# Kernel optimization log

Measured on AMD Instinct MI355X. Metric: run time of the kernel, lower is better.

Reference implementation:

```python
import jax, jax.numpy as jnp
import numpy as np

L, B, S, D, H, DH, V = 6, 2048, 64, 256, 8, 64, 100
INNER = H * DH          # 512
FF = 4 * D              # 1024 (GeGLU hidden after chunk)
SCALE = 8.0             # sqrt(DH)


def setup_inputs() -> dict:
    key = jax.random.key(0)
    ks = jax.random.split(key, 8)
    s = 0.02
    return {
        "x": jax.random.randint(ks[0], (B, S), 0, V),
        "E": jax.random.normal(ks[1], (S, V, D), dtype=jnp.float32) * s,
        "ln1_g": jnp.ones((L, D), jnp.float32),
        "ln1_b": jnp.zeros((L, D), jnp.float32),
        "Wqkv": jax.random.normal(ks[2], (L, D, 3 * INNER), dtype=jnp.float32) * s,
        "Wout": jax.random.normal(ks[3], (L, INNER, D), dtype=jnp.float32) * s,
        "bout": jnp.zeros((L, D), jnp.float32),
        "ln2_g": jnp.ones((L, D), jnp.float32),
        "ln2_b": jnp.zeros((L, D), jnp.float32),
        "W1": jax.random.normal(ks[4], (L, D, 2 * FF), dtype=jnp.float32) * s,
        "b1": jnp.zeros((L, 2 * FF), jnp.float32),
        "W2": jax.random.normal(ks[5], (L, FF, D), dtype=jnp.float32) * s,
        "b2": jnp.zeros((L, D), jnp.float32),
    }


def _ln(x, g, b):
    m = x.mean(-1, keepdims=True)
    v = ((x - m) ** 2).mean(-1, keepdims=True)
    return (x - m) * jax.lax.rsqrt(v + 1e-5) * g + b


def _split_heads(t):
    # [B,S,H*DH] -> [B,H,S,DH]
    return t.reshape(B, S, H, DH).transpose(0, 2, 1, 3)


def reference(x, E, ln1_g, ln1_b, Wqkv, Wout, bout, ln2_g, ln2_b, W1, b1, W2, b2):
    # per-column embedding lookup: E[col, x[b,col]] -> [B,S,D]
    h = E[jnp.arange(S)[None, :], x]
    for l in range(L):
        # PreNorm -> MHA
        n = _ln(h, ln1_g[l], ln1_b[l])
        qkv = n @ Wqkv[l]
        q, k, v = jnp.split(qkv, 3, axis=-1)
        q, k, v = _split_heads(q), _split_heads(k), _split_heads(v)
        score = jax.nn.softmax(
            jnp.einsum("bhqd,bhkd->bhqk", q, k) / SCALE, axis=-1
        )
        o = jnp.einsum("bhqk,bhkd->bhqd", score, v)
        o = o.transpose(0, 2, 1, 3).reshape(B, S, INNER)
        h = h + o @ Wout[l] + bout[l]
        # PreNorm -> GeGLU FFN
        n2 = _ln(h, ln2_g[l], ln2_b[l])
        u = n2 @ W1[l] + b1[l]
        a, g = jnp.split(u, 2, axis=-1)
        h = (a * jax.nn.gelu(g, approximate=False)) @ W2[l] + b2[l] + h
    return h
```

## Files before the change

### kernel.cpp

```cpp
#include <hip/hip_runtime.h>
#include <stdint.h>
#include <math.h>


#define LAYERS 6
#define BATCH  2048
#define SEQ    64
#define DMODEL 256
#define NHEAD  8
#define INNERD 512
#define FFDIM  1024
#define VOCAB  100
#define MTOK   (BATCH*SEQ)

typedef unsigned short u16;
typedef __attribute__((ext_vector_type(4))) float f32x4;
typedef __attribute__((ext_vector_type(4))) short s16x4;
typedef __attribute__((ext_vector_type(8))) short s16x8;

__device__ inline u16 f2bf(float f){
  union { float f; unsigned int u; } x; x.f = f;
  unsigned int u = x.u;
  return (u16)((u + 0x7fffu + ((u >> 16) & 1u)) >> 16);
}

__device__ inline void gload16(const void* g, void* l){
  __builtin_amdgcn_global_load_lds(
      (const __attribute__((address_space(1))) unsigned int*)g,
      (__attribute__((address_space(3))) unsigned int*)l, 16, 0, 0);
}

__device__ inline f32x4 mfma16(s16x8 a, s16x8 b, f32x4 c){
  return __builtin_amdgcn_mfma_f32_16x16x32_bf16(a, b, c, 0, 0, 0);
}

__device__ inline s16x8 ldfrag(const u16* lds, int row, int kk, int g){
  int chunk = ((kk<<2)|g) ^ (row&7);
  return *(const s16x8*)(lds + row*64 + chunk*8);
}

__device__ inline int pcol32(int col_base32, int hi, int g, int o){
  return col_base32 | (g<<3) | (hi<<2) | o;
}

__global__ __launch_bounds__(256) void wtrans_kernel(
    const float* __restrict__ in, u16* __restrict__ out, int K, int N, int total)
{
  int idx = blockIdx.x*256 + threadIdx.x;
  if (idx >= total) return;
  int l = idx / (N*K);
  int r = idx - l*(N*K);
  int n = r / K;
  int k = r - n*K;
  int p = (k & ~31) | (((k>>2)&3)<<3) | (((k>>4)&1)<<2) | (k&3);
  out[(size_t)l*N*K + (size_t)n*K + p] = f2bf(in[(size_t)l*K*N + (size_t)k*N + n]);
}

__global__ __launch_bounds__(256) void embed_ln_kernel(
    const int* __restrict__ x, const float* __restrict__ E,
    const float* __restrict__ gam, const float* __restrict__ bet,
    float* __restrict__ h, u16* __restrict__ nout)
{
  int t = threadIdx.x;
  int m = blockIdx.x*4 + (t>>6);
  int lane = t & 63;
  int s = m & 63;
  int tok = x[m];
  const float4 v = *(const float4*)(E + ((size_t)s*VOCAB + tok)*DMODEL + lane*4);
  *(float4*)(h + (size_t)m*DMODEL + lane*4) = v;
  float su = v.x+v.y+v.z+v.w;
  float q  = v.x*v.x+v.y*v.y+v.z*v.z+v.w*v.w;
  #pragma unroll
  for (int mask=1; mask<64; mask<<=1){
    su += __shfl_xor(su, mask);
    q  += __shfl_xor(q,  mask);
  }
  float mean = su*(1.f/256.f);
  float var  = q*(1.f/256.f) - mean*mean;
  float rs   = rsqrtf(var + 1e-5f);
  const float4 gv = *(const float4*)(gam + lane*4);
  const float4 bv = *(const float4*)(bet + lane*4);
  ushort4 ov;
  ov.x = f2bf((v.x-mean)*rs*gv.x + bv.x);
  ov.y = f2bf((v.y-mean)*rs*gv.y + bv.y);
  ov.z = f2bf((v.z-mean)*rs*gv.z + bv.z);
  ov.w = f2bf((v.w-mean)*rs*gv.w + bv.w);
  int p4 = (lane>>3)*32 + (lane&3)*8 + ((lane>>2)&1)*4;
  *(ushort4*)(nout + (size_t)m*DMODEL + p4) = ov;
}

__global__ __launch_bounds__(256, 2) void gemm_qkv_kernel(
    const u16* __restrict__ A, const u16* __restrict__ Bt,
    u16* __restrict__ outb, int K, int N)
{
  __shared__ __align__(16) u16 As[128*64];
  __shared__ __align__(16) u16 Bs[128*64];
  const int t = threadIdx.x;
  const int w = t >> 6, lane = t & 63, g = lane >> 4, c = lane & 15;
  const int nxb = N >> 7;
  const int cpx = gridDim.x >> 3;
  const int wg = (blockIdx.x & 7)*cpx + (blockIdx.x >> 3);
  const int n0 = (wg % nxb) * 128, m0 = (wg / nxb) * 128;
  const int wm = (w >> 1) * 64, wn = (w & 1) * 64;

  f32x4 acc[4][4];
  #pragma unroll
  for (int i=0;i<4;++i)
    #pragma unroll
    for (int j=0;j<4;++j){ f32x4 z = {0.f,0.f,0.f,0.f}; acc[i][j] = z; }

  const int nkt = K >> 6;
  for (int kt = 0; kt < nkt; ++kt){
    #pragma unroll
    for (int i=0;i<4;++i){
      int cid = (i*4 + w)*64 + lane;
      int row = cid >> 3, qs = cid & 7;
      int col16 = ((qs ^ (row&7))<<3);
      gload16(A  + (size_t)(m0+row)*K + (size_t)kt*64 + col16, As + (i*4+w)*512);
      gload16(Bt + (size_t)(n0+row)*K + (size_t)kt*64 + col16, Bs + (i*4+w)*512);
    }
    asm volatile("s_waitcnt vmcnt(0)" ::: "memory");
    __syncthreads();
    #pragma unroll
    for (int kk=0; kk<2; ++kk){
      s16x8 af[4];
      #pragma unroll
      for (int i=0;i<4;++i) af[i] = ldfrag(As, wm + i*16 + c, kk, g);
      #pragma unroll
      for (int j=0;j<4;++j){
        s16x8 bf = ldfrag(Bs, wn + j*16 + c, kk, g);
        #pragma unroll
        for (int i=0;i<4;++i) acc[i][j] = mfma16(af[i], bf, acc[i][j]);
      }
    }
    __syncthreads();
  }

  #pragma unroll
  for (int i=0;i<4;++i)
    #pragma unroll
    for (int j=0;j<4;++j){
      int col = n0 + wn + j*16 + c;
      #pragma unroll
      for (int r=0;r<4;++r){
        int m = m0 + wm + i*16 + g*4 + r;
        outb[(size_t)m*N + col] = f2bf(acc[i][j][r]);
      }
    }
}

__global__ __launch_bounds__(256, 2) void gemm_gated_kernel(
    const u16* __restrict__ A, const u16* __restrict__ Bt,
    u16* __restrict__ act, const float* __restrict__ b1, int K)
{
  __shared__ __align__(16) u16 As[128*64];
  __shared__ __align__(16) u16 Ba[128*64];
  __shared__ __align__(16) u16 Bg[128*64];
  const int t = threadIdx.x;
  const int w = t >> 6, lane = t & 63, g = lane >> 4, c = lane & 15;
  const int cpx = gridDim.x >> 3;
  const int wg = (blockIdx.x & 7)*cpx + (blockIdx.x >> 3);
  const int n0 = (wg & 7) * 128, m0 = (wg >> 3) * 128;
  const int wm = (w >> 1) * 64, wn = (w & 1) * 64;

  f32x4 acca[4][4], accg[4][4];
  #pragma unroll
  for (int i=0;i<4;++i)
    #pragma unroll
    for (int j=0;j<4;++j){ f32x4 z = {0.f,0.f,0.f,0.f}; acca[i][j] = z; accg[i][j] = z; }

  const int nkt = K >> 6;
  for (int kt = 0; kt < nkt; ++kt){
    #pragma unroll
    for (int i=0;i<4;++i){
      int cid = (i*4 + w)*64 + lane;
      int row = cid >> 3, qs = cid & 7;
      int col16 = ((qs ^ (row&7))<<3);
      gload16(A  + (size_t)(m0+row)*K      + (size_t)kt*64 + col16, As + (i*4+w)*512);
      gload16(Bt + (size_t)(n0+row)*K      + (size_t)kt*64 + col16, Ba + (i*4+w)*512);
      gload16(Bt + (size_t)(1024+n0+row)*K + (size_t)kt*64 + col16, Bg + (i*4+w)*512);
    }
    asm volatile("s_waitcnt vmcnt(0)" ::: "memory");
    __syncthreads();
    #pragma unroll
    for (int kk=0; kk<2; ++kk){
      s16x8 af[4];
      #pragma unroll
      for (int i=0;i<4;++i) af[i] = ldfrag(As, wm + i*16 + c, kk, g);
      #pragma unroll
      for (int j=0;j<4;++j){
        int row = wn + j*16 + c;
        s16x8 bfa = ldfrag(Ba, row, kk, g);
        s16x8 bfg = ldfrag(Bg, row, kk, g);
        #pragma unroll
        for (int i=0;i<4;++i){
          acca[i][j] = mfma16(af[i], bfa, acca[i][j]);
          accg[i][j] = mfma16(af[i], bfg, accg[i][j]);
        }
      }
    }
    __syncthreads();
  }

  #pragma unroll
  for (int i=0;i<4;++i)
    #pragma unroll
    for (int j=0;j<4;++j){
      int col = n0 + wn + j*16 + c;
      int pc = pcol32(col & ~31, j&1, c>>2, c&3);
      float ba = b1[col], bg = b1[1024 + col];
      #pragma unroll
      for (int r=0;r<4;++r){
        int m = m0 + wm + i*16 + g*4 + r;
        float ua = acca[i][j][r] + ba;
        float ug = accg[i][j][r] + bg;
        float gel = 0.5f*ug*(1.0f + erff(ug*0.70710678118654752f));
        act[(size_t)m*FFDIM + pc] = f2bf(ua*gel);
      }
    }
}

template<int DO_LN>
__global__ __launch_bounds__(256, 2) void gemm_res_ln_kernel(
    const u16* __restrict__ A, const u16* __restrict__ Bt,
    float* __restrict__ h, const float* __restrict__ bias,
    const float* __restrict__ gam, const float* __restrict__ bet,
    u16* __restrict__ nout, int K)
{
  __shared__ __align__(16) u16 As[128*64];
  __shared__ __align__(16) u16 Bs[256*64];
  __shared__ float ps[128][4];
  const int t = threadIdx.x;
  const int w = t >> 6, lane = t & 63, g = lane >> 4, c = lane & 15;
  const int wr = w >> 1, wc = w & 1;
  const int m0 = blockIdx.x * 128;

  f32x4 acc[4][8];
  #pragma unroll
  for (int i=0;i<4;++i)
    #pragma unroll
    for (int j=0;j<8;++j){ f32x4 z = {0.f,0.f,0.f,0.f}; acc[i][j] = z; }

  const int nkt = K >> 6;
  for (int kt = 0; kt < nkt; ++kt){
    #pragma unroll
    for (int i=0;i<4;++i){
      int cid = (i*4 + w)*64 + lane;
      int row = cid >> 3, qs = cid & 7;
      gload16(A + (size_t)(m0+row)*K + (size_t)kt*64 + ((qs ^ (row&7))<<3),
              As + (i*4+w)*512);
    }
    #pragma unroll
    for (int i=0;i<8;++i){
      int cid = (i*4 + w)*64 + lane;
      int row = cid >> 3, qs = cid & 7;
      gload16(Bt + (size_t)row*K + (size_t)kt*64 + ((qs ^ (row&7))<<3),
              Bs + (i*4+w)*512);
    }
    asm volatile("s_waitcnt vmcnt(0)" ::: "memory");
    __syncthreads();
    #pragma unroll
    for (int kk=0; kk<2; ++kk){
      s16x8 af[4];
      #pragma unroll
      for (int i=0;i<4;++i) af[i] = ldfrag(As, wr*64 + i*16 + c, kk, g);
      #pragma unroll
      for (int j=0;j<8;++j){
        s16x8 bf = ldfrag(Bs, wc*128 + j*16 + c, kk, g);
        #pragma unroll
        for (int i=0;i<4;++i) acc[i][j] = mfma16(af[i], bf, acc[i][j]);
      }
    }
    __syncthreads();
  }

  #pragma unroll
  for (int i=0;i<4;++i){
    #pragma unroll
    for (int r=0;r<4;++r){
      int rl = wr*64 + i*16 + g*4 + r;
      size_t mrow = (size_t)(m0 + rl)*DMODEL;
      float s = 0.f, q2 = 0.f;
      #pragma unroll
      for (int j=0;j<8;++j){
        int col = wc*128 + j*16 + c;
        float v = acc[i][j][r] + bias[col] + h[mrow + col];
        h[mrow + col] = v;
        s += v; q2 += v*v;
      }
      if (DO_LN){
        #pragma unroll
        for (int mask=1; mask<16; mask<<=1){
          s  += __shfl_xor(s,  mask);
          q2 += __shfl_xor(q2, mask);
        }
        if (c == 0){ ps[rl][wc*2] = s; ps[rl][wc*2+1] = q2; }
      }
    }
  }
  if (DO_LN){
    __syncthreads();
    #pragma unroll
    for (int i=0;i<4;++i){
      #pragma unroll
      for (int r=0;r<4;++r){
        int rl = wr*64 + i*16 + g*4 + r;
        size_t mrow = (size_t)(m0 + rl)*DMODEL;
        float st = ps[rl][0] + ps[rl][2];
        float qt = ps[rl][1] + ps[rl][3];
        float mean = st*(1.f/256.f);
        float var  = qt*(1.f/256.f) - mean*mean;
        float rs   = rsqrtf(var + 1e-5f);
        #pragma unroll
        for (int j=0;j<8;++j){
          int col = wc*128 + j*16 + c;
          float v = h[mrow + col];
          int pc = pcol32(col & ~31, j&1, c>>2, c&3);
          nout[mrow + pc] = f2bf((v-mean)*rs*gam[col] + bet[col]);
        }
      }
    }
  }
}

__global__ __launch_bounds__(256) void attn_kernel(
    const u16* __restrict__ qkv, u16* __restrict__ o)
{
  __shared__ __align__(16) u16 qs[64*72];
  __shared__ __align__(16) u16 ks[64*72];
  __shared__ __align__(16) u16 vt[64*72];
  __shared__ __align__(16) u16 psm[4*16*72];
  const int t = threadIdx.x;
  const int w = t >> 6, lane = t & 63, g = lane >> 4, c = lane & 15;
  const int bh = blockIdx.x, b = bh >> 3, hh = bh & 7;
  const size_t qbase = (size_t)b*64*1536 + hh*64;

  #pragma unroll
  for (int i=0;i<2;++i){
    int cid = i*256 + t;
    int row = cid >> 3, seg = cid & 7;
    size_t go = qbase + (size_t)row*1536 + seg*8;
    *(uint4*)(&qs[row*72 + seg*8]) = *(const uint4*)(qkv + go);
    *(uint4*)(&ks[row*72 + seg*8]) = *(const uint4*)(qkv + go + 512);
    uint4 vv = *(const uint4*)(qkv + go + 1024);
    const u16* pv = (const u16*)&vv;
    #pragma unroll
    for (int j=0;j<8;++j) vt[(seg*8+j)*72 + row] = pv[j];
  }
  __syncthreads();

  f32x4 accS[4];
  #pragma unroll
  for (int nf=0;nf<4;++nf){ f32x4 z = {0.f,0.f,0.f,0.f}; accS[nf] = z; }
  const int arow = w*16 + c;
  #pragma unroll
  for (int kk=0;kk<2;++kk){
    int k0 = kk*32 + 4*g;
    s16x4 alo = *(const s16x4*)(qs + arow*72 + k0);
    s16x4 ahi = *(const s16x4*)(qs + arow*72 + k0 + 16);
    s16x8 a = __builtin_shufflevector(alo, ahi, 0,1,2,3,4,5,6,7);
    #pragma unroll
    for (int nf=0;nf<4;++nf){
      int brow = nf*16 + c;
      s16x4 blo = *(const s16x4*)(ks + brow*72 + k0);
      s16x4 bhi = *(const s16x4*)(ks + brow*72 + k0 + 16);
      s16x8 bb = __builtin_shufflevector(blo, bhi, 0,1,2,3,4,5,6,7);
      accS[nf] = mfma16(a, bb, accS[nf]);
    }
  }

  u16* pw = psm + w*16*72;
  #pragma unroll
  for (int r=0;r<4;++r){
    float mx = fmaxf(fmaxf(accS[0][r],accS[1][r]), fmaxf(accS[2][r],accS[3][r]));
    #pragma unroll
    for (int mask=1; mask<16; mask<<=1) mx = fmaxf(mx, __shfl_xor(mx, mask));
    float p0 = expf((accS[0][r]-mx)*0.125f);
    float p1 = expf((accS[1][r]-mx)*0.125f);
    float p2 = expf((accS[2][r]-mx)*0.125f);
    float p3 = expf((accS[3][r]-mx)*0.125f);
    float sm = p0+p1+p2+p3;
    #pragma unroll
    for (int mask=1; mask<16; mask<<=1) sm += __shfl_xor(sm, mask);
    float inv = 1.f/sm;
    pw[(g*4+r)*72 +  0 + c] = f2bf(p0*inv);
    pw[(g*4+r)*72 + 16 + c] = f2bf(p1*inv);
    pw[(g*4+r)*72 + 32 + c] = f2bf(p2*inv);
    pw[(g*4+r)*72 + 48 + c] = f2bf(p3*inv);
  }
  __syncthreads();

  f32x4 accO[4];
  #pragma unroll
  for (int nf=0;nf<4;++nf){ f32x4 z = {0.f,0.f,0.f,0.f}; accO[nf] = z; }
  #pragma unroll
  for (int kk=0;kk<2;++kk){
    int k0 = kk*32 + 4*g;
    s16x4 alo = *(const s16x4*)(pw + c*72 + k0);
    s16x4 ahi = *(const s16x4*)(pw + c*72 + k0 + 16);
    s16x8 a = __builtin_shufflevector(alo, ahi, 0,1,2,3,4,5,6,7);
    #pragma unroll
    for (int nf=0;nf<4;++nf){
      int brow = nf*16 + c;
      s16x4 blo = *(const s16x4*)(vt + brow*72 + k0);
      s16x4 bhi = *(const s16x4*)(vt + brow*72 + k0 + 16);
      s16x8 bb = __builtin_shufflevector(blo, bhi, 0,1,2,3,4,5,6,7);
      accO[nf] = mfma16(a, bb, accO[nf]);
    }
  }

  #pragma unroll
  for (int nf=0;nf<4;++nf){
    #pragma unroll
    for (int r=0;r<4;++r){
      int q = w*16 + g*4 + r;
      int col = hh*64 + nf*16 + c;
      int pc = pcol32(col & ~31, nf&1, c>>2, c&3);
      o[(size_t)(b*64 + q)*INNERD + pc] = f2bf(accO[nf][r]);
    }
  }
}

extern "C" void kernel_launch(void* const* d_in, const int* in_sizes, int n_in,
                              void* d_out, int out_size, void* d_ws, size_t ws_size,
                              hipStream_t stream)
{
  const int*   x    = (const int*)  d_in[0];
  const float* E    = (const float*)d_in[1];
  const float* ln1g = (const float*)d_in[2];
  const float* ln1b = (const float*)d_in[3];
  const float* Wqkv = (const float*)d_in[4];
  const float* Wout = (const float*)d_in[5];
  const float* bout = (const float*)d_in[6];
  const float* ln2g = (const float*)d_in[7];
  const float* ln2b = (const float*)d_in[8];
  const float* W1   = (const float*)d_in[9];
  const float* b1   = (const float*)d_in[10];
  const float* W2   = (const float*)d_in[11];
  const float* b2   = (const float*)d_in[12];
  float* h = (float*)d_out;

  const size_t WQKV = (size_t)LAYERS*1536*256;
  const size_t WOUT = (size_t)LAYERS*256*512;
  const size_t W1T  = (size_t)LAYERS*2048*256;
  const size_t W2T  = (size_t)LAYERS*256*1024;
  u16* wqkv_t = (u16*)d_ws;
  u16* wout_t = wqkv_t + WQKV;
  u16* w1_t   = wout_t + WOUT;
  u16* w2_t   = w1_t   + W1T;
  u16* abase  = w2_t   + W2T;
  const size_t wbytes = (WQKV + WOUT + W1T + W2T) * 2;
  if (ws_size < wbytes + (size_t)1024*4608) return;
  size_t rem = ws_size - wbytes;

  int Mc = MTOK;
  while (Mc > 1024 && (size_t)Mc*4608 > rem) Mc >>= 1;
  const int nc = MTOK / Mc;

  u16* n_bf   = abase;
  u16* o_bf   = n_bf + (size_t)Mc*256;
  u16* qkv_bf = o_bf + (size_t)Mc*512;
  u16* act_bf = qkv_bf;

  int tot;
  tot = LAYERS*1536*256; wtrans_kernel<<<(tot+255)/256,256,0,stream>>>(Wqkv, wqkv_t, 256,  1536, tot);
  tot = LAYERS*256*512;  wtrans_kernel<<<(tot+255)/256,256,0,stream>>>(Wout, wout_t, 512,  256,  tot);
  tot = LAYERS*2048*256; wtrans_kernel<<<(tot+255)/256,256,0,stream>>>(W1,   w1_t,   256,  2048, tot);
  tot = LAYERS*256*1024; wtrans_kernel<<<(tot+255)/256,256,0,stream>>>(W2,   w2_t,   1024, 256,  tot);

  for (int cidx=0; cidx<nc; ++cidx){
    float* hc = h + (size_t)cidx*Mc*256;
    const int* xc = x + (size_t)cidx*Mc;
    embed_ln_kernel<<<Mc/4,256,0,stream>>>(xc, E, ln1g, ln1b, hc, n_bf);
    for (int l=0; l<LAYERS; ++l){
      gemm_qkv_kernel<<<12*(Mc/128),256,0,stream>>>(
          n_bf, wqkv_t + (size_t)l*1536*256, qkv_bf, 256, 1536);
      attn_kernel<<<(Mc/64)*NHEAD,256,0,stream>>>(qkv_bf, o_bf);
      gemm_res_ln_kernel<1><<<Mc/128,256,0,stream>>>(
          o_bf, wout_t + (size_t)l*256*512, hc, bout + l*256,
          ln2g + l*256, ln2b + l*256, n_bf, 512);
      gemm_gated_kernel<<<8*(Mc/128),256,0,stream>>>(
          n_bf, w1_t + (size_t)l*2048*256, act_bf, b1 + l*2048, 256);
      if (l < LAYERS-1){
        gemm_res_ln_kernel<1><<<Mc/128,256,0,stream>>>(
            act_bf, w2_t + (size_t)l*256*1024, hc, b2 + l*256,
            ln1g + (l+1)*256, ln1b + (l+1)*256, n_bf, 1024);
      } else {
        gemm_res_ln_kernel<0><<<Mc/128,256,0,stream>>>(
            act_bf, w2_t + (size_t)l*256*1024, hc, b2 + l*256,
            nullptr, nullptr, nullptr, 1024);
      }
    }
  }
}
```

Before: 4.503 ms.

## Fuse QKV projection GEMM with per-head attention in one kernel

Replaces the separate QKV GEMM and attention kernels with one kernel. Each block computes Q, K and V for one head over 128 tokens (two sequences), writes them to LDS (V transposed), then runs softmax attention directly from LDS. This removes the global write and re-read of the full QKV tensor and one launch per layer, and shrinks the workspace so larger token chunks fit. In exchange the kernel uses about 76KB of LDS, which may limit occupancy below the requested two blocks per CU, and it launches fewer blocks.

After: 4.582 ms. Within noise of the previous version (+1.8%).

```diff
diff --git a/kernel.cpp b/kernel.cpp
--- a/kernel.cpp
+++ b/kernel.cpp
@@ -37,6 +37,12 @@
 __device__ inline s16x8 ldfrag(const u16* lds, int row, int kk, int g){
   int chunk = ((kk<<2)|g) ^ (row&7);
   return *(const s16x8*)(lds + row*64 + chunk*8);
+}
+
+__device__ inline s16x8 frag2(const u16* p){
+  s16x4 lo = *(const s16x4*)(p);
+  s16x4 hi = *(const s16x4*)(p + 16);
+  return __builtin_shufflevector(lo, hi, 0,1,2,3,4,5,6,7);
 }
 
 __device__ inline int pcol32(int col_base32, int hi, int g, int o){
@@ -89,64 +95,161 @@
   *(ushort4*)(nout + (size_t)m*DMODEL + p4) = ov;
 }
 
-__global__ __launch_bounds__(256, 2) void gemm_qkv_kernel(
+__global__ __launch_bounds__(256, 2) void qkv_attn_kernel(
     const u16* __restrict__ A, const u16* __restrict__ Bt,
-    u16* __restrict__ outb, int K, int N)
-{
-  __shared__ __align__(16) u16 As[128*64];
-  __shared__ __align__(16) u16 Bs[128*64];
+    u16* __restrict__ o, int K)
+{
+  __shared__ __align__(16) u16 smem[38912];
+  u16* As = smem;
+  u16* Bs = smem + 8192;
+  u16* qs = smem;
+  u16* ks = smem + 9216;
+  u16* vt = smem + 20480;
+  u16* ps = smem + 29696;
+
   const int t = threadIdx.x;
   const int w = t >> 6, lane = t & 63, g = lane >> 4, c = lane & 15;
-  const int nxb = N >> 7;
   const int cpx = gridDim.x >> 3;
   const int wg = (blockIdx.x & 7)*cpx + (blockIdx.x >> 3);
-  const int n0 = (wg % nxb) * 128, m0 = (wg / nxb) * 128;
-  const int wm = (w >> 1) * 64, wn = (w & 1) * 64;
-
-  f32x4 acc[4][4];
-  #pragma unroll
-  for (int i=0;i<4;++i)
-    #pragma unroll
-    for (int j=0;j<4;++j){ f32x4 z = {0.f,0.f,0.f,0.f}; acc[i][j] = z; }
+  const int hh = wg & 7;
+  const int m0 = (wg >> 3) * 128;
+
+  f32x4 acc[2][12];
+  #pragma unroll
+  for (int i=0;i<2;++i)
+    #pragma unroll
+    for (int j=0;j<12;++j){ f32x4 z = {0.f,0.f,0.f,0.f}; acc[i][j] = z; }
 
   const int nkt = K >> 6;
   for (int kt = 0; kt < nkt; ++kt){
     #pragma unroll
     for (int i=0;i<4;++i){
       int cid = (i*4 + w)*64 + lane;
-      int row = cid >> 3, qs = cid & 7;
-      int col16 = ((qs ^ (row&7))<<3);
-      gload16(A  + (size_t)(m0+row)*K + (size_t)kt*64 + col16, As + (i*4+w)*512);
-      gload16(Bt + (size_t)(n0+row)*K + (size_t)kt*64 + col16, Bs + (i*4+w)*512);
+      int row = cid >> 3, seg = cid & 7;
+      gload16(A + (size_t)(m0+row)*K + (size_t)kt*64 + ((seg ^ (row&7))<<3),
+              As + cid*8);
+    }
+    #pragma unroll
+    for (int i=0;i<6;++i){
+      int cid = (i*4 + w)*64 + lane;
+      int brow = cid >> 3, seg = cid & 7;
+      int ng = (brow>>6)*512 + hh*64 + (brow & 63);
+      gload16(Bt + (size_t)ng*K + (size_t)kt*64 + ((seg ^ (brow&7))<<3),
+              Bs + cid*8);
     }
     asm volatile("s_waitcnt vmcnt(0)" ::: "memory");
     __syncthreads();
     #pragma unroll
     for (int kk=0; kk<2; ++kk){
-      s16x8 af[4];
-      #pragma unroll
-      for (int i=0;i<4;++i) af[i] = ldfrag(As, wm + i*16 + c, kk, g);
-      #pragma unroll
-      for (int j=0;j<4;++j){
-        s16x8 bf = ldfrag(Bs, wn + j*16 + c, kk, g);
-        #pragma unroll
-        for (int i=0;i<4;++i) acc[i][j] = mfma16(af[i], bf, acc[i][j]);
-      }
-    }
-    __syncthreads();
-  }
-
-  #pragma unroll
-  for (int i=0;i<4;++i)
+      s16x8 af[2];
+      #pragma unroll
+      for (int i=0;i<2;++i) af[i] = ldfrag(As, w*32 + i*16 + c, kk, g);
+      #pragma unroll
+      for (int j=0;j<12;++j){
+        s16x8 bf = ldfrag(Bs, j*16 + c, kk, g);
+        acc[0][j] = mfma16(af[0], bf, acc[0][j]);
+        acc[1][j] = mfma16(af[1], bf, acc[1][j]);
+      }
+    }
+    __syncthreads();
+  }
+
+  #pragma unroll
+  for (int i=0;i<2;++i){
+    #pragma unroll
+    for (int j=0;j<12;++j){
+      int col = j*16 + c;
+      #pragma unroll
+      for (int r=0;r<4;++r){
+        int tl = w*32 + i*16 + g*4 + r;
+        u16 val = f2bf(acc[i][j][r]);
+        if (j < 4)       qs[tl*72 + col] = val;
+        else if (j < 8)  ks[tl*72 + (col - 64)] = val;
+        else             vt[((tl & 64) + col - 128)*72 + (tl & 63)] = val;
+      }
+    }
+  }
+  __syncthreads();
+
+  const int seq = w >> 1;
+  const u16* qb = qs + (w*32)*72;
+  const u16* kb = ks + (seq*64)*72;
+  const u16* vb = vt + (seq*64)*72;
+  u16* pw = ps + (w*32)*72;
+
+  f32x4 sc[2][4];
+  #pragma unroll
+  for (int i=0;i<2;++i)
+    #pragma unroll
+    for (int j=0;j<4;++j){ f32x4 z = {0.f,0.f,0.f,0.f}; sc[i][j] = z; }
+  #pragma unroll
+  for (int kk=0;kk<2;++kk){
+    int k0 = kk*32 + 4*g;
+    s16x8 a0 = frag2(qb + (c)*72      + k0);
+    s16x8 a1 = frag2(qb + (16 + c)*72 + k0);
     #pragma unroll
     for (int j=0;j<4;++j){
-      int col = n0 + wn + j*16 + c;
+      s16x8 bb = frag2(kb + (j*16 + c)*72 + k0);
+      sc[0][j] = mfma16(a0, bb, sc[0][j]);
+      sc[1][j] = mfma16(a1, bb, sc[1][j]);
+    }
+  }
+
+  #pragma unroll
+  for (int i=0;i<2;++i){
+    #pragma unroll
+    for (int r=0;r<4;++r){
+      float mx = fmaxf(fmaxf(sc[i][0][r],sc[i][1][r]), fmaxf(sc[i][2][r],sc[i][3][r]));
+      #pragma unroll
+      for (int mask=1; mask<16; mask<<=1) mx = fmaxf(mx, __shfl_xor(mx, mask));
+      float p0 = expf((sc[i][0][r]-mx)*0.125f);
+      float p1 = expf((sc[i][1][r]-mx)*0.125f);
+      float p2 = expf((sc[i][2][r]-mx)*0.125f);
+      float p3 = expf((sc[i][3][r]-mx)*0.125f);
+      float sm = p0+p1+p2+p3;
+      #pragma unroll
+      for (int mask=1; mask<16; mask<<=1) sm += __shfl_xor(sm, mask);
+      float inv = 1.f/sm;
+      int row = i*16 + g*4 + r;
+      pw[row*72 +  0 + c] = f2bf(p0*inv);
+      pw[row*72 + 16 + c] = f2bf(p1*inv);
+      pw[row*72 + 32 + c] = f2bf(p2*inv);
+      pw[row*72 + 48 + c] = f2bf(p3*inv);
+    }
+  }
+  __syncthreads();
+
+  f32x4 oa[2][4];
+  #pragma unroll
+  for (int i=0;i<2;++i)
+    #pragma unroll
+    for (int j=0;j<4;++j){ f32x4 z = {0.f,0.f,0.f,0.f}; oa[i][j] = z; }
+  #pragma unroll
+  for (int kk=0;kk<2;++kk){
+    int k0 = kk*32 + 4*g;
+    s16x8 a0 = frag2(pw + (c)*72      + k0);
+    s16x8 a1 = frag2(pw + (16 + c)*72 + k0);
+    #pragma unroll
+    for (int j=0;j<4;++j){
+      s16x8 bb = frag2(vb + (j*16 + c)*72 + k0);
+      oa[0][j] = mfma16(a0, bb, oa[0][j]);
+      oa[1][j] = mfma16(a1, bb, oa[1][j]);
+    }
+  }
+
+  #pragma unroll
+  for (int i=0;i<2;++i){
+    #pragma unroll
+    for (int j=0;j<4;++j){
+      int col = hh*64 + j*16 + c;
+      int pc = pcol32(col & ~31, j&1, c>>2, c&3);
       #pragma unroll
       for (int r=0;r<4;++r){
-        int m = m0 + wm + i*16 + g*4 + r;
-        outb[(size_t)m*N + col] = f2bf(acc[i][j][r]);
-      }
-    }
+        int m = m0 + w*32 + i*16 + g*4 + r;
+        o[(size_t)m*INNERD + pc] = f2bf(oa[i][j][r]);
+      }
+    }
+  }
 }
 
 __global__ __launch_bounds__(256, 2) void gemm_gated_kernel(
@@ -323,104 +426,6 @@
   }
 }
 
-__global__ __launch_bounds__(256) void attn_kernel(
-    const u16* __restrict__ qkv, u16* __restrict__ o)
-{
-  __shared__ __align__(16) u16 qs[64*72];
-  __shared__ __align__(16) u16 ks[64*72];
-  __shared__ __align__(16) u16 vt[64*72];
-  __shared__ __align__(16) u16 psm[4*16*72];
-  const int t = threadIdx.x;
-  const int w = t >> 6, lane = t & 63, g = lane >> 4, c = lane & 15;
-  const int bh = blockIdx.x, b = bh >> 3, hh = bh & 7;
-  const size_t qbase = (size_t)b*64*1536 + hh*64;
-
-  #pragma unroll
-  for (int i=0;i<2;++i){
-    int cid = i*256 + t;
-    int row = cid >> 3, seg = cid & 7;
-    size_t go = qbase + (size_t)row*1536 + seg*8;
-    *(uint4*)(&qs[row*72 + seg*8]) = *(const uint4*)(qkv + go);
-    *(uint4*)(&ks[row*72 + seg*8]) = *(const uint4*)(qkv + go + 512);
-    uint4 vv = *(const uint4*)(qkv + go + 1024);
-    const u16* pv = (const u16*)&vv;
-    #pragma unroll
-    for (int j=0;j<8;++j) vt[(seg*8+j)*72 + row] = pv[j];
-  }
-  __syncthreads();
-
-  f32x4 accS[4];
-  #pragma unroll
-  for (int nf=0;nf<4;++nf){ f32x4 z = {0.f,0.f,0.f,0.f}; accS[nf] = z; }
-  const int arow = w*16 + c;
-  #pragma unroll
-  for (int kk=0;kk<2;++kk){
-    int k0 = kk*32 + 4*g;
-    s16x4 alo = *(const s16x4*)(qs + arow*72 + k0);
-    s16x4 ahi = *(const s16x4*)(qs + arow*72 + k0 + 16);
-    s16x8 a = __builtin_shufflevector(alo, ahi, 0,1,2,3,4,5,6,7);
-    #pragma unroll
-    for (int nf=0;nf<4;++nf){
-      int brow = nf*16 + c;
-      s16x4 blo = *(const s16x4*)(ks + brow*72 + k0);
-      s16x4 bhi = *(const s16x4*)(ks + brow*72 + k0 + 16);
-      s16x8 bb = __builtin_shufflevector(blo, bhi, 0,1,2,3,4,5,6,7);
-      accS[nf] = mfma16(a, bb, accS[nf]);
-    }
-  }
-
-  u16* pw = psm + w*16*72;
-  #pragma unroll
-  for (int r=0;r<4;++r){
-    float mx = fmaxf(fmaxf(accS[0][r],accS[1][r]), fmaxf(accS[2][r],accS[3][r]));
-    #pragma unroll
-    for (int mask=1; mask<16; mask<<=1) mx = fmaxf(mx, __shfl_xor(mx, mask));
-    float p0 = expf((accS[0][r]-mx)*0.125f);
-    float p1 = expf((accS[1][r]-mx)*0.125f);
-    float p2 = expf((accS[2][r]-mx)*0.125f);
-    float p3 = expf((accS[3][r]-mx)*0.125f);
-    float sm = p0+p1+p2+p3;
-    #pragma unroll
-    for (int mask=1; mask<16; mask<<=1) sm += __shfl_xor(sm, mask);
-    float inv = 1.f/sm;
-    pw[(g*4+r)*72 +  0 + c] = f2bf(p0*inv);
-    pw[(g*4+r)*72 + 16 + c] = f2bf(p1*inv);
-    pw[(g*4+r)*72 + 32 + c] = f2bf(p2*inv);
-    pw[(g*4+r)*72 + 48 + c] = f2bf(p3*inv);
-  }
-  __syncthreads();
-
-  f32x4 accO[4];
-  #pragma unroll
-  for (int nf=0;nf<4;++nf){ f32x4 z = {0.f,0.f,0.f,0.f}; accO[nf] = z; }
-  #pragma unroll
-  for (int kk=0;kk<2;++kk){
-    int k0 = kk*32 + 4*g;
-    s16x4 alo = *(const s16x4*)(pw + c*72 + k0);
-    s16x4 ahi = *(const s16x4*)(pw + c*72 + k0 + 16);
-    s16x8 a = __builtin_shufflevector(alo, ahi, 0,1,2,3,4,5,6,7);
-    #pragma unroll
-    for (int nf=0;nf<4;++nf){
-      int brow = nf*16 + c;
-      s16x4 blo = *(const s16x4*)(vt + brow*72 + k0);
-      s16x4 bhi = *(const s16x4*)(vt + brow*72 + k0 + 16);
-      s16x8 bb = __builtin_shufflevector(blo, bhi, 0,1,2,3,4,5,6,7);
-      accO[nf] = mfma16(a, bb, accO[nf]);
-    }
-  }
-
-  #pragma unroll
-  for (int nf=0;nf<4;++nf){
-    #pragma unroll
-    for (int r=0;r<4;++r){
-      int q = w*16 + g*4 + r;
-      int col = hh*64 + nf*16 + c;
-      int pc = pcol32(col & ~31, nf&1, c>>2, c&3);
-      o[(size_t)(b*64 + q)*INNERD + pc] = f2bf(accO[nf][r]);
-    }
-  }
-}
-
 extern "C" void kernel_launch(void* const* d_in, const int* in_sizes, int n_in,
                               void* d_out, int out_size, void* d_ws, size_t ws_size,
                               hipStream_t stream)
@@ -450,17 +455,16 @@
   u16* w2_t   = w1_t   + W1T;
   u16* abase  = w2_t   + W2T;
   const size_t wbytes = (WQKV + WOUT + W1T + W2T) * 2;
-  if (ws_size < wbytes + (size_t)1024*4608) return;
+  if (ws_size < wbytes + (size_t)1024*3584) return;
   size_t rem = ws_size - wbytes;
 
   int Mc = MTOK;
-  while (Mc > 1024 && (size_t)Mc*4608 > rem) Mc >>= 1;
+  while (Mc > 1024 && (size_t)Mc*3584 > rem) Mc >>= 1;
   const int nc = MTOK / Mc;
 
   u16* n_bf   = abase;
   u16* o_bf   = n_bf + (size_t)Mc*256;
-  u16* qkv_bf = o_bf + (size_t)Mc*512;
-  u16* act_bf = qkv_bf;
+  u16* act_bf = o_bf + (size_t)Mc*512;
 
   int tot;
   tot = LAYERS*1536*256; wtrans_kernel<<<(tot+255)/256,256,0,stream>>>(Wqkv, wqkv_t, 256,  1536, tot);
@@ -473,9 +477,8 @@
     const int* xc = x + (size_t)cidx*Mc;
     embed_ln_kernel<<<Mc/4,256,0,stream>>>(xc, E, ln1g, ln1b, hc, n_bf);
     for (int l=0; l<LAYERS; ++l){
-      gemm_qkv_kernel<<<12*(Mc/128),256,0,stream>>>(
-          n_bf, wqkv_t + (size_t)l*1536*256, qkv_bf, 256, 1536);
-      attn_kernel<<<(Mc/64)*NHEAD,256,0,stream>>>(qkv_bf, o_bf);
+      qkv_attn_kernel<<<8*(Mc/128),256,0,stream>>>(
+          n_bf, wqkv_t + (size_t)l*1536*256, o_bf, 256);
       gemm_res_ln_kernel<1><<<Mc/128,256,0,stream>>>(
           o_bf, wout_t + (size_t)l*256*512, hc, bout + l*256,
           ln2g + l*256, ln2b + l*256, n_bf, 512);
```
